# Kernel tuning notes

Hardware: AMD Instinct MI355X
Metric: run time of the kernel (lower is better)

The kernel has to match this reference:

```python
import jax, jax.numpy as jnp
import numpy as np

N_NODES = 100_000
N_EDGES = 1_600_000
D_IN = 128
D_HID = 64   # hard-coded hidden width in Embedder.__init__
D_OUT = 128  # embed_dim
N_GRAPHS = 512


def setup_inputs() -> dict:
    key = jax.random.key(0)
    ks = jax.random.split(key, 10)
    x = jax.random.normal(ks[0], (N_NODES, D_IN), dtype=jnp.float32)
    edge_index = jax.random.randint(ks[1], (2, N_EDGES), 0, N_NODES, dtype=jnp.int64)
    batch_index = jnp.sort(jax.random.randint(ks[2], (N_NODES,), 0, N_GRAPHS, dtype=jnp.int64))
    def glorot(k, fan_in, fan_out):
        s = 1.0 / np.sqrt(fan_in)
        return jax.random.uniform(k, (fan_in, fan_out), jnp.float32, -s, s)
    # layer 1: SAGEConv(D_IN -> D_HID); layer 2: SAGEConv(D_HID -> D_OUT)
    return {
        "x": x,
        "W1_l": glorot(ks[3], D_IN, D_HID),   # applied to mean-aggregated neighbors
        "W1_r": glorot(ks[4], D_IN, D_HID),   # applied to root node
        "b1": jnp.zeros((D_HID,), jnp.float32),
        "W2_l": glorot(ks[5], D_HID, D_OUT),
        "W2_r": glorot(ks[6], D_HID, D_OUT),
        "b2": jnp.zeros((D_OUT,), jnp.float32),
        "edge_index": edge_index,
        "batch_index": batch_index,
    }


def _sage_conv(x, edge_index, W_l, W_r, b):
    # PyG SAGEConv with mean aggregation:
    # out_i = (mean_{j in N(i)} x_j) @ W_l + x_i @ W_r + b
    src, dst = edge_index[0], edge_index[1]
    n = x.shape[0]
    agg = jax.ops.segment_sum(x[src], dst, num_segments=n)          # [N, F]
    deg = jax.ops.segment_sum(jnp.ones((src.shape[0],), x.dtype), dst, num_segments=n)
    mean_nbr = agg / jnp.maximum(deg, 1.0)[:, None]
    return mean_nbr @ W_l + x @ W_r + b


def reference(x, W1_l, W1_r, b1, W2_l, W2_r, b2, edge_index, batch_index):
    h = _sage_conv(x, edge_index, W1_l, W1_r, b1)
    h = jax.nn.relu(h)
    h = _sage_conv(h, edge_index, W2_l, W2_r, b2)
    # F.dropout(p=0.5, training=False) -> identity in eval mode
    # gap: global mean pool per graph
    sums = jax.ops.segment_sum(h, batch_index, num_segments=N_GRAPHS)
    cnts = jax.ops.segment_sum(jnp.ones((h.shape[0],), h.dtype), batch_index, num_segments=N_GRAPHS)
    return sums / jnp.maximum(cnts, 1.0)[:, None]
```

## Files before the change

kernel.cpp:

```cpp
#include <hip/hip_runtime.h>

#define NN   100000
#define NE   1600000
#define DIN  128
#define DH   64
#define DOUT 128
#define NG   512

#define NB   391
#define EPB  6250
#define CAP  5120

typedef short short8 __attribute__((ext_vector_type(8)));
typedef float floatx4 __attribute__((ext_vector_type(4)));

__device__ __forceinline__ unsigned short f2bf(float f) {
  unsigned b = __float_as_uint(f);
  b += 0x7FFF + ((b >> 16) & 1);
  return (unsigned short)(b >> 16);
}
__device__ __forceinline__ float bflo(unsigned u) {
  return __uint_as_float(u << 16);
}
__device__ __forceinline__ float bfhi(unsigned u) {
  return __uint_as_float(u & 0xFFFF0000u);
}
__device__ __forceinline__ unsigned pack2(float a, float b) {
  return (unsigned)f2bf(a) | ((unsigned)f2bf(b) << 16);
}

__global__ __launch_bounds__(256) void prep_kernel(
    int* __restrict__ gcur,
    const float* __restrict__ W1l, const float* __restrict__ W1r,
    short* __restrict__ wfrag, const int* __restrict__ batch,
    int* __restrict__ gs) {
  int b = blockIdx.x;
  if (b == 0) {
    for (int i = threadIdx.x; i < NB; i += 256) gcur[i] = i * CAP;
  } else if (b == 1) {
    for (int i = threadIdx.x; i < DIN * DH; i += 256) {
      int k = i >> 6, n = i & 63;
      int kt = k >> 5, kin = k & 31;
      int lane = ((kin >> 3) << 4) | (n & 15);
      int j8 = kin & 7;
      int jt = n >> 4;
      float wl = W1l[i], wr = W1r[i];
      unsigned bl_ = __float_as_uint(wl);
      unsigned br_ = __float_as_uint(wr);
      short hl = (short)(bl_ >> 16);
      short hr = (short)(br_ >> 16);
      float rl = wl - __uint_as_float(bl_ & 0xFFFF0000u);
      float rr = wr - __uint_as_float(br_ & 0xFFFF0000u);
      short ll = (short)(__float_as_uint(rl) >> 16);
      short lr = (short)(__float_as_uint(rr) >> 16);
      int base0 = (((kt * 2 + 0) * 4 + jt) * 2) * 512 + lane * 8 + j8;
      int base1 = (((kt * 2 + 1) * 4 + jt) * 2) * 512 + lane * 8 + j8;
      wfrag[base0]       = hl;
      wfrag[base0 + 512] = ll;
      wfrag[base1]       = hr;
      wfrag[base1 + 512] = lr;
    }
  } else {
    for (int g = threadIdx.x; g <= NG; g += 256) {
      if (g == NG) { gs[NG] = NN; continue; }
      int lo = 0, hi = NN;
      while (lo < hi) {
        int mid = (lo + hi) >> 1;
        if (batch[mid] < g) lo = mid + 1; else hi = mid;
      }
      gs[g] = lo;
    }
  }
}

__global__ __launch_bounds__(256, 4) void proj_part_kernel(
    const int* __restrict__ src, const int* __restrict__ dst,
    int* __restrict__ gcur, int* __restrict__ part,
    const float* __restrict__ x, const short* __restrict__ wfrag,
    const float* __restrict__ b1, unsigned short* __restrict__ xlb,
    unsigned short* __restrict__ xrb) {
  __shared__ short sB[16384];
  if (blockIdx.x < 256) {
    int* hist  = (int*)sB;
    int* base_ = hist + NB;
    int* lcur  = hist + 2 * NB;
    for (int i = threadIdx.x; i < NB; i += 256) hist[i] = 0;
    __syncthreads();
    int start = blockIdx.x * EPB, end = start + EPB;
    for (int e = start + threadIdx.x; e < end; e += 256)
      atomicAdd(&hist[dst[e] >> 8], 1);
    __syncthreads();
    for (int i = threadIdx.x; i < NB; i += 256) {
      base_[i] = atomicAdd(&gcur[i], hist[i]);
      lcur[i] = 0;
    }
    __syncthreads();
    for (int e = start + threadIdx.x; e < end; e += 256) {
      int d = dst[e], s = src[e];
      int bkt = d >> 8;
      int pos = base_[bkt] + atomicAdd(&lcur[bkt], 1);
      if (pos < (bkt + 1) * CAP)
        part[pos] = ((d & 255) << 17) | s;
    }
    return;
  }
  int wave = threadIdx.x >> 6;
  int lane = threadIdx.x & 63;
  int m = lane & 15, q = lane >> 4;
  int tpair = (blockIdx.x - 256) * 4 + wave;
  int tile0 = tpair * 2, tile1 = tile0 + 1;
  bool act0 = tile0 < 6250;
  bool act1 = tile1 < 6250;
  int t0c = act0 ? tile0 : 6249;
  int t1c = act1 ? tile1 : 6249;

  int r0 = t0c * 16 + m;
  int r1 = t1c * 16 + m;
  const float4* xa = (const float4*)x + (size_t)r0 * 32 + q * 2;
  const float4* xb = (const float4*)x + (size_t)r1 * 32 + q * 2;

  floatx4 acc0[8], acc1[8];
#pragma unroll
  for (int a = 0; a < 8; ++a) {
    acc0[a] = (floatx4){0.f, 0.f, 0.f, 0.f};
    acc1[a] = (floatx4){0.f, 0.f, 0.f, 0.f};
  }

  const float4* wf4 = (const float4*)wfrag;
  float4* sB4 = (float4*)sB;

#pragma unroll 1
  for (int stage = 0; stage < 2; ++stage) {
    if (stage) __syncthreads();
    for (int i = threadIdx.x; i < 2048; i += 256)
      sB4[i] = wf4[stage * 2048 + i];
    __syncthreads();

#pragma unroll
    for (int kk = 0; kk < 2; ++kk) {
      int kt = stage * 2 + kk;
      float4 p0 = xa[kt * 8];
      float4 p1 = xa[kt * 8 + 1];
      float4 p2 = xb[kt * 8];
      float4 p3 = xb[kt * 8 + 1];
      float af0[8] = {p0.x, p0.y, p0.z, p0.w, p1.x, p1.y, p1.z, p1.w};
      float af1[8] = {p2.x, p2.y, p2.z, p2.w, p3.x, p3.y, p3.z, p3.w};
      short8 ah0, al0, ah1, al1;
#pragma unroll
      for (int e = 0; e < 8; ++e) {
        unsigned b0 = __float_as_uint(af0[e]);
        ah0[e] = (short)(b0 >> 16);
        float lo0 = af0[e] - __uint_as_float(b0 & 0xFFFF0000u);
        al0[e] = (short)(__float_as_uint(lo0) >> 16);
        unsigned b1_ = __float_as_uint(af1[e]);
        ah1[e] = (short)(b1_ >> 16);
        float lo1 = af1[e] - __uint_as_float(b1_ & 0xFFFF0000u);
        al1[e] = (short)(__float_as_uint(lo1) >> 16);
      }
#pragma unroll
      for (int mat = 0; mat < 2; ++mat) {
#pragma unroll
        for (int jt = 0; jt < 4; ++jt) {
          int unit = ((kk * 2 + mat) * 4 + jt) * 2;
          short8 bh = *(const short8*)(sB + unit * 512 + lane * 8);
          short8 bl = *(const short8*)(sB + (unit + 1) * 512 + lane * 8);
          floatx4 c0 = acc0[mat * 4 + jt];
          c0 = __builtin_amdgcn_mfma_f32_16x16x32_bf16(ah0, bh, c0, 0, 0, 0);
          c0 = __builtin_amdgcn_mfma_f32_16x16x32_bf16(ah0, bl, c0, 0, 0, 0);
          c0 = __builtin_amdgcn_mfma_f32_16x16x32_bf16(al0, bh, c0, 0, 0, 0);
          acc0[mat * 4 + jt] = c0;
          floatx4 c1 = acc1[mat * 4 + jt];
          c1 = __builtin_amdgcn_mfma_f32_16x16x32_bf16(ah1, bh, c1, 0, 0, 0);
          c1 = __builtin_amdgcn_mfma_f32_16x16x32_bf16(ah1, bl, c1, 0, 0, 0);
          c1 = __builtin_amdgcn_mfma_f32_16x16x32_bf16(al1, bh, c1, 0, 0, 0);
          acc1[mat * 4 + jt] = c1;
        }
      }
    }
  }

#pragma unroll
  for (int jt = 0; jt < 4; ++jt) {
    int j = jt * 16 + m;
    float bj = b1[j];
    floatx4 cl0 = acc0[jt], cr0 = acc0[4 + jt];
    floatx4 cl1 = acc1[jt], cr1 = acc1[4 + jt];
    if (act0) {
#pragma unroll
      for (int r = 0; r < 4; ++r) {
        int n0 = tile0 * 16 + q * 4 + r;
        xlb[(size_t)n0 * DH + j] = f2bf(cl0[r]);
        xrb[(size_t)n0 * DH + j] = f2bf(cr0[r] + bj);
      }
    }
    if (act1) {
#pragma unroll
      for (int r = 0; r < 4; ++r) {
        int n1 = tile1 * 16 + q * 4 + r;
        xlb[(size_t)n1 * DH + j] = f2bf(cl1[r]);
        xrb[(size_t)n1 * DH + j] = f2bf(cr1[r] + bj);
      }
    }
  }
}

__global__ __launch_bounds__(256) void bucket_csr_kernel(
    const int* __restrict__ part, const int* __restrict__ gcur,
    int* __restrict__ row_start, int* __restrict__ row_end,
    int* __restrict__ eidx) {
  int b = blockIdx.x, t = threadIdx.x;
  int ebeg = b * CAP;
  int cnt_b = gcur[b] - ebeg; if (cnt_b > CAP) cnt_b = CAP;
  int eend = ebeg + cnt_b;
  int nbase = b << 8;
  int nloc = NN - nbase; if (nloc > 256) nloc = 256;
  __shared__ int cntL[256];
  __shared__ int exclL[256];
  cntL[t] = 0;
  __syncthreads();
  for (int e = ebeg + t; e < eend; e += 256)
    atomicAdd(&cntL[part[e] >> 17], 1);
  __syncthreads();
  int c = cntL[t];
  exclL[t] = c;
  __syncthreads();
  for (int off = 1; off < 256; off <<= 1) {
    int v = (t >= off) ? exclL[t - off] : 0;
    __syncthreads();
    exclL[t] += v;
    __syncthreads();
  }
  int excl = exclL[t] - c;
  if (t < nloc) {
    row_start[nbase + t] = ebeg + excl;
    row_end[nbase + t]   = ebeg + excl + c;
  }
  cntL[t] = excl;
  __syncthreads();
  for (int e = ebeg + t; e < eend; e += 256) {
    int v = part[e];
    int pos = atomicAdd(&cntL[v >> 17], 1);
    eidx[ebeg + pos] = v & 0x1FFFF;
  }
}

template <bool RELU_ADD>
__global__ __launch_bounds__(256) void gather_kernel(
    const uint4* __restrict__ feat4, const int* __restrict__ row_start,
    const int* __restrict__ row_end, const int* __restrict__ eidx,
    const uint4* __restrict__ xr4, uint4* __restrict__ out4) {
  int t = blockIdx.x * 256 + threadIdx.x;
  int node = t >> 3;
  if (node >= NN) return;
  int fl = t & 7;
  int rs = row_start[node], re = row_end[node];
  float a0 = 0.f, a1 = 0.f, a2 = 0.f, a3 = 0.f;
  float a4 = 0.f, a5 = 0.f, a6 = 0.f, a7 = 0.f;
  int k = rs;
  for (; k + 8 <= re; k += 8) {
    uint4 v[8];
#pragma unroll
    for (int u = 0; u < 8; ++u) v[u] = feat4[(size_t)eidx[k + u] * 8 + fl];
#pragma unroll
    for (int u = 0; u < 8; ++u) {
      a0 += bflo(v[u].x); a1 += bfhi(v[u].x);
      a2 += bflo(v[u].y); a3 += bfhi(v[u].y);
      a4 += bflo(v[u].z); a5 += bfhi(v[u].z);
      a6 += bflo(v[u].w); a7 += bfhi(v[u].w);
    }
  }
  for (; k + 2 <= re; k += 2) {
    uint4 v0 = feat4[(size_t)eidx[k] * 8 + fl];
    uint4 v1 = feat4[(size_t)eidx[k + 1] * 8 + fl];
    a0 += bflo(v0.x) + bflo(v1.x); a1 += bfhi(v0.x) + bfhi(v1.x);
    a2 += bflo(v0.y) + bflo(v1.y); a3 += bfhi(v0.y) + bfhi(v1.y);
    a4 += bflo(v0.z) + bflo(v1.z); a5 += bfhi(v0.z) + bfhi(v1.z);
    a6 += bflo(v0.w) + bflo(v1.w); a7 += bfhi(v0.w) + bfhi(v1.w);
  }
  if (k < re) {
    uint4 v = feat4[(size_t)eidx[k] * 8 + fl];
    a0 += bflo(v.x); a1 += bfhi(v.x);
    a2 += bflo(v.y); a3 += bfhi(v.y);
    a4 += bflo(v.z); a5 += bfhi(v.z);
    a6 += bflo(v.w); a7 += bfhi(v.w);
  }
  float inv = 1.0f / fmaxf((float)(re - rs), 1.0f);
  a0 *= inv; a1 *= inv; a2 *= inv; a3 *= inv;
  a4 *= inv; a5 *= inv; a6 *= inv; a7 *= inv;
  if (RELU_ADD) {
    uint4 r = xr4[(size_t)node * 8 + fl];
    a0 = fmaxf(a0 + bflo(r.x), 0.f); a1 = fmaxf(a1 + bfhi(r.x), 0.f);
    a2 = fmaxf(a2 + bflo(r.y), 0.f); a3 = fmaxf(a3 + bfhi(r.y), 0.f);
    a4 = fmaxf(a4 + bflo(r.z), 0.f); a5 = fmaxf(a5 + bfhi(r.z), 0.f);
    a6 = fmaxf(a6 + bflo(r.w), 0.f); a7 = fmaxf(a7 + bfhi(r.w), 0.f);
  }
  uint4 o;
  o.x = pack2(a0, a1);
  o.y = pack2(a2, a3);
  o.z = pack2(a4, a5);
  o.w = pack2(a6, a7);
  out4[(size_t)node * 8 + fl] = o;
}

__global__ __launch_bounds__(1024) void gather2_pool_kernel(
    const uint4* __restrict__ feat4,
    const int* __restrict__ row_start, const int* __restrict__ row_end,
    const int* __restrict__ eidx,
    const int* __restrict__ gs, const float* __restrict__ W2l,
    const float* __restrict__ W2r, const float* __restrict__ b2,
    float* __restrict__ out) {
  int g = blockIdx.x;
  int start = gs[g], end = gs[g + 1];
  int slot = threadIdx.x >> 3;
  int fl   = threadIdx.x & 7;
  float sm[8], sh[8];
#pragma unroll
  for (int i = 0; i < 8; ++i) { sm[i] = 0.f; sh[i] = 0.f; }

  for (int n = start + slot; n < end; n += 128) {
    int rs = row_start[n], re = row_end[n];
    float a0 = 0.f, a1 = 0.f, a2 = 0.f, a3 = 0.f;
    float a4 = 0.f, a5 = 0.f, a6 = 0.f, a7 = 0.f;
    int k = rs;
    for (; k + 4 <= re; k += 4) {
      uint4 v[4];
#pragma unroll
      for (int u = 0; u < 4; ++u) v[u] = feat4[(size_t)eidx[k + u] * 8 + fl];
#pragma unroll
      for (int u = 0; u < 4; ++u) {
        a0 += bflo(v[u].x); a1 += bfhi(v[u].x);
        a2 += bflo(v[u].y); a3 += bfhi(v[u].y);
        a4 += bflo(v[u].z); a5 += bfhi(v[u].z);
        a6 += bflo(v[u].w); a7 += bfhi(v[u].w);
      }
    }
    for (; k < re; ++k) {
      uint4 v = feat4[(size_t)eidx[k] * 8 + fl];
      a0 += bflo(v.x); a1 += bfhi(v.x);
      a2 += bflo(v.y); a3 += bfhi(v.y);
      a4 += bflo(v.z); a5 += bfhi(v.z);
      a6 += bflo(v.w); a7 += bfhi(v.w);
    }
    float inv = 1.0f / fmaxf((float)(re - rs), 1.0f);
    sm[0] += a0 * inv; sm[1] += a1 * inv; sm[2] += a2 * inv; sm[3] += a3 * inv;
    sm[4] += a4 * inv; sm[5] += a5 * inv; sm[6] += a6 * inv; sm[7] += a7 * inv;
    uint4 hv = feat4[(size_t)n * 8 + fl];
    sh[0] += bflo(hv.x); sh[1] += bfhi(hv.x);
    sh[2] += bflo(hv.y); sh[3] += bfhi(hv.y);
    sh[4] += bflo(hv.z); sh[5] += bfhi(hv.z);
    sh[6] += bflo(hv.w); sh[7] += bfhi(hv.w);
  }

#pragma unroll
  for (int off = 8; off <= 32; off <<= 1) {
#pragma unroll
    for (int i = 0; i < 8; ++i) {
      sm[i] += __shfl_xor(sm[i], off);
      sh[i] += __shfl_xor(sh[i], off);
    }
  }

  __shared__ float redm[16][DH];
  __shared__ float redh[16][DH];
  int wv = threadIdx.x >> 6;
  int lane = threadIdx.x & 63;
  if (lane < 8) {
#pragma unroll
    for (int i = 0; i < 8; ++i) {
      redm[wv][lane * 8 + i] = sm[i];
      redh[wv][lane * 8 + i] = sh[i];
    }
  }
  __syncthreads();
  __shared__ float msL[DH], hsL[DH];
  if (threadIdx.x < DH) {
    float a = 0.f, b = 0.f;
#pragma unroll
    for (int w = 0; w < 16; ++w) { a += redm[w][threadIdx.x]; b += redh[w][threadIdx.x]; }
    msL[threadIdx.x] = a; hsL[threadIdx.x] = b;
  }
  __syncthreads();
  int j = threadIdx.x;
  if (j < DOUT) {
    float n_ = (float)(end - start);
    float acc = 0.f;
#pragma unroll 8
    for (int k = 0; k < DH; ++k)
      acc += msL[k] * W2l[k * DOUT + j] + hsL[k] * W2r[k * DOUT + j];
    out[g * DOUT + j] = (acc + n_ * b2[j]) / fmaxf(n_, 1.0f);
  }
}

extern "C" void kernel_launch(void* const* d_in, const int* in_sizes, int n_in,
                              void* d_out, int out_size, void* d_ws, size_t ws_size,
                              hipStream_t stream) {
  (void)in_sizes; (void)n_in; (void)out_size; (void)ws_size;
  const float* x   = (const float*)d_in[0];
  const float* W1l = (const float*)d_in[1];
  const float* W1r = (const float*)d_in[2];
  const float* b1  = (const float*)d_in[3];
  const float* W2l = (const float*)d_in[4];
  const float* W2r = (const float*)d_in[5];
  const float* b2  = (const float*)d_in[6];
  const int*   ei  = (const int*)d_in[7];
  const int*   batch = (const int*)d_in[8];
  const int* src = ei;
  const int* dst = ei + NE;
  float* out = (float*)d_out;

  char* ws = (char*)d_ws;
  unsigned short* xlb = (unsigned short*)(ws);
  unsigned short* hb  = (unsigned short*)(ws + 12800000);
  unsigned short* xrb = (unsigned short*)(ws + 38400000);
  int*  part      = (int*)(ws + 51200000);
  int*  gcur      = (int*)(ws + 59300000);
  int*  eidx      = (int*)(ws + 60000000);
  int*  row_start = (int*)(ws + 83200000);
  int*   gs       = (int*)(ws + 83600128);
  short* wfrag    = (short*)(ws + 83900032);
  int*  row_end   = (int*)(ws + 84000000);

  const int gBlocks = (NN * 8 + 255) / 256;

  prep_kernel<<<3, 256, 0, stream>>>(gcur, W1l, W1r, wfrag, batch, gs);

  proj_part_kernel<<<1038, 256, 0, stream>>>(src, dst, gcur, part,
                                             x, wfrag, b1, xlb, xrb);
  bucket_csr_kernel<<<NB, 256, 0, stream>>>(part, gcur, row_start, row_end, eidx);

  gather_kernel<true><<<gBlocks, 256, 0, stream>>>(
      (const uint4*)xlb, row_start, row_end, eidx, (const uint4*)xrb, (uint4*)hb);

  gather2_pool_kernel<<<NG, 1024, 0, stream>>>(
      (const uint4*)hb, row_start, row_end, eidx, gs, W2l, W2r, b2, out);
}
```

Measured before the change: 239.5 us.

## Read projection weights directly from global memory and use one tile per wave

```diff
diff --git a/kernel.cpp b/kernel.cpp
--- a/kernel.cpp
+++ b/kernel.cpp
@@ -79,11 +79,11 @@
     const float* __restrict__ x, const short* __restrict__ wfrag,
     const float* __restrict__ b1, unsigned short* __restrict__ xlb,
     unsigned short* __restrict__ xrb) {
-  __shared__ short sB[16384];
+  __shared__ int sH[3 * NB];
   if (blockIdx.x < 256) {
-    int* hist  = (int*)sB;
-    int* base_ = hist + NB;
-    int* lcur  = hist + 2 * NB;
+    int* hist  = sH;
+    int* base_ = sH + NB;
+    int* lcur  = sH + 2 * NB;
     for (int i = threadIdx.x; i < NB; i += 256) hist[i] = 0;
     __syncthreads();
     int start = blockIdx.x * EPB, end = start + EPB;
@@ -107,98 +107,58 @@
   int wave = threadIdx.x >> 6;
   int lane = threadIdx.x & 63;
   int m = lane & 15, q = lane >> 4;
-  int tpair = (blockIdx.x - 256) * 4 + wave;
-  int tile0 = tpair * 2, tile1 = tile0 + 1;
-  bool act0 = tile0 < 6250;
-  bool act1 = tile1 < 6250;
-  int t0c = act0 ? tile0 : 6249;
-  int t1c = act1 ? tile1 : 6249;
-
-  int r0 = t0c * 16 + m;
-  int r1 = t1c * 16 + m;
+  int tile = (blockIdx.x - 256) * 4 + wave;
+  bool act = tile < 6250;
+  int tc = act ? tile : 6249;
+
+  int r0 = tc * 16 + m;
   const float4* xa = (const float4*)x + (size_t)r0 * 32 + q * 2;
-  const float4* xb = (const float4*)x + (size_t)r1 * 32 + q * 2;
-
-  floatx4 acc0[8], acc1[8];
-#pragma unroll
-  for (int a = 0; a < 8; ++a) {
-    acc0[a] = (floatx4){0.f, 0.f, 0.f, 0.f};
-    acc1[a] = (floatx4){0.f, 0.f, 0.f, 0.f};
-  }
-
-  const float4* wf4 = (const float4*)wfrag;
-  float4* sB4 = (float4*)sB;
-
-#pragma unroll 1
-  for (int stage = 0; stage < 2; ++stage) {
-    if (stage) __syncthreads();
-    for (int i = threadIdx.x; i < 2048; i += 256)
-      sB4[i] = wf4[stage * 2048 + i];
-    __syncthreads();
-
-#pragma unroll
-    for (int kk = 0; kk < 2; ++kk) {
-      int kt = stage * 2 + kk;
-      float4 p0 = xa[kt * 8];
-      float4 p1 = xa[kt * 8 + 1];
-      float4 p2 = xb[kt * 8];
-      float4 p3 = xb[kt * 8 + 1];
-      float af0[8] = {p0.x, p0.y, p0.z, p0.w, p1.x, p1.y, p1.z, p1.w};
-      float af1[8] = {p2.x, p2.y, p2.z, p2.w, p3.x, p3.y, p3.z, p3.w};
-      short8 ah0, al0, ah1, al1;
-#pragma unroll
-      for (int e = 0; e < 8; ++e) {
-        unsigned b0 = __float_as_uint(af0[e]);
-        ah0[e] = (short)(b0 >> 16);
-        float lo0 = af0[e] - __uint_as_float(b0 & 0xFFFF0000u);
-        al0[e] = (short)(__float_as_uint(lo0) >> 16);
-        unsigned b1_ = __float_as_uint(af1[e]);
-        ah1[e] = (short)(b1_ >> 16);
-        float lo1 = af1[e] - __uint_as_float(b1_ & 0xFFFF0000u);
-        al1[e] = (short)(__float_as_uint(lo1) >> 16);
+  const short8* wf = (const short8*)wfrag + lane;
+
+  floatx4 acc[8];
+#pragma unroll
+  for (int a = 0; a < 8; ++a) acc[a] = (floatx4){0.f, 0.f, 0.f, 0.f};
+
+#pragma unroll
+  for (int kt = 0; kt < 4; ++kt) {
+    float4 p0 = xa[kt * 8];
+    float4 p1 = xa[kt * 8 + 1];
+    float af0[8] = {p0.x, p0.y, p0.z, p0.w, p1.x, p1.y, p1.z, p1.w};
+    short8 ah, al;
+#pragma unroll
+    for (int e = 0; e < 8; ++e) {
+      unsigned b0 = __float_as_uint(af0[e]);
+      ah[e] = (short)(b0 >> 16);
+      float lo0 = af0[e] - __uint_as_float(b0 & 0xFFFF0000u);
+      al[e] = (short)(__float_as_uint(lo0) >> 16);
+    }
+#pragma unroll
+    for (int mat = 0; mat < 2; ++mat) {
+#pragma unroll
+      for (int jt = 0; jt < 4; ++jt) {
+        int unit = ((kt * 2 + mat) * 4 + jt) * 2;
+        short8 bh = wf[unit * 64];
+        short8 bl = wf[unit * 64 + 64];
+        floatx4 c = acc[mat * 4 + jt];
+        c = __builtin_amdgcn_mfma_f32_16x16x32_bf16(ah, bh, c, 0, 0, 0);
+        c = __builtin_amdgcn_mfma_f32_16x16x32_bf16(ah, bl, c, 0, 0, 0);
+        c = __builtin_amdgcn_mfma_f32_16x16x32_bf16(al, bh, c, 0, 0, 0);
+        acc[mat * 4 + jt] = c;
       }
-#pragma unroll
-      for (int mat = 0; mat < 2; ++mat) {
-#pragma unroll
-        for (int jt = 0; jt < 4; ++jt) {
-          int unit = ((kk * 2 + mat) * 4 + jt) * 2;
-          short8 bh = *(const short8*)(sB + unit * 512 + lane * 8);
-          short8 bl = *(const short8*)(sB + (unit + 1) * 512 + lane * 8);
-          floatx4 c0 = acc0[mat * 4 + jt];
-          c0 = __builtin_amdgcn_mfma_f32_16x16x32_bf16(ah0, bh, c0, 0, 0, 0);
-          c0 = __builtin_amdgcn_mfma_f32_16x16x32_bf16(ah0, bl, c0, 0, 0, 0);
-          c0 = __builtin_amdgcn_mfma_f32_16x16x32_bf16(al0, bh, c0, 0, 0, 0);
-          acc0[mat * 4 + jt] = c0;
-          floatx4 c1 = acc1[mat * 4 + jt];
-          c1 = __builtin_amdgcn_mfma_f32_16x16x32_bf16(ah1, bh, c1, 0, 0, 0);
-          c1 = __builtin_amdgcn_mfma_f32_16x16x32_bf16(ah1, bl, c1, 0, 0, 0);
-          c1 = __builtin_amdgcn_mfma_f32_16x16x32_bf16(al1, bh, c1, 0, 0, 0);
-          acc1[mat * 4 + jt] = c1;
-        }
-      }
-    }
-  }
-
-#pragma unroll
-  for (int jt = 0; jt < 4; ++jt) {
-    int j = jt * 16 + m;
-    float bj = b1[j];
-    floatx4 cl0 = acc0[jt], cr0 = acc0[4 + jt];
-    floatx4 cl1 = acc1[jt], cr1 = acc1[4 + jt];
-    if (act0) {
+    }
+  }
+
+  if (act) {
+#pragma unroll
+    for (int jt = 0; jt < 4; ++jt) {
+      int j = jt * 16 + m;
+      float bj = b1[j];
+      floatx4 cl = acc[jt], cr = acc[4 + jt];
 #pragma unroll
       for (int r = 0; r < 4; ++r) {
-        int n0 = tile0 * 16 + q * 4 + r;
-        xlb[(size_t)n0 * DH + j] = f2bf(cl0[r]);
-        xrb[(size_t)n0 * DH + j] = f2bf(cr0[r] + bj);
-      }
-    }
-    if (act1) {
-#pragma unroll
-      for (int r = 0; r < 4; ++r) {
-        int n1 = tile1 * 16 + q * 4 + r;
-        xlb[(size_t)n1 * DH + j] = f2bf(cl1[r]);
-        xrb[(size_t)n1 * DH + j] = f2bf(cr1[r] + bj);
+        int n0 = tile * 16 + q * 4 + r;
+        xlb[(size_t)n0 * DH + j] = f2bf(cl[r]);
+        xrb[(size_t)n0 * DH + j] = f2bf(cr[r] + bj);
       }
     }
   }
@@ -424,8 +384,8 @@
 
   prep_kernel<<<3, 256, 0, stream>>>(gcur, W1l, W1r, wfrag, batch, gs);
 
-  proj_part_kernel<<<1038, 256, 0, stream>>>(src, dst, gcur, part,
-                                             x, wfrag, b1, xlb, xrb);
+  proj_part_kernel<<<256 + 1563, 256, 0, stream>>>(src, dst, gcur, part,
+                                                   x, wfrag, b1, xlb, xrb);
   bucket_csr_kernel<<<NB, 256, 0, stream>>>(part, gcur, row_start, row_end, eidx);
 
   gather_kernel<true><<<gBlocks, 256, 0, stream>>>(
```

Measured after the change: 249.4 us. 1.04x slower.
